# Performance work log

Measured on AMD Instinct MI355X. Metric: run time of the kernel, lower is better.

## Reference

```python
import jax, jax.numpy as jnp
import numpy as np

N = 100000
E = 1600000
F_IN = 256   # 4 * 64 after concat
H = 128

def _glorot(key, shape):
    fan_in, fan_out = shape
    lim = jnp.sqrt(6.0 / (fan_in + fan_out))
    return jax.random.uniform(key, shape, jnp.float32, -lim, lim)

def setup_inputs() -> dict:
    key = jax.random.key(0)
    ks = jax.random.split(key, 32)
    inp = {
        'x': jax.random.normal(ks[0], (N, 64), jnp.float32),
        'diff': jax.random.normal(ks[1], (N, 64), jnp.float32),
        'rec_prev': jax.random.normal(ks[2], (N, 64), jnp.float32),
        'hidden_prev': jax.random.normal(ks[3], (N, 64), jnp.float32),
        'edge_index': jax.random.randint(ks[4], (2, E), 0, N, jnp.int64),
    }
    dims = [(F_IN, H), (H, H), (H, H), (H, 1)]
    for i, (din, dout) in enumerate(dims):
        inp[f'Wl{i}'] = _glorot(ks[5 + 3 * i], (din, dout))  # neighbor (aggr) weight
        inp[f'Wr{i}'] = _glorot(ks[6 + 3 * i], (din, dout))  # root weight
        inp[f'b{i}'] = jnp.zeros((dout,), jnp.float32)
    return inp

def _sage_conv(h, src, dst, Wl, Wr, b):
    # mean aggregation of source-node features at destination nodes (PyG SAGEConv)
    msg_sum = jax.ops.segment_sum(h[src], dst, num_segments=N)        # [N, F]
    cnt = jax.ops.segment_sum(jnp.ones((src.shape[0],), h.dtype), dst, num_segments=N)
    mean = msg_sum / jnp.maximum(cnt, 1.0)[:, None]
    return mean @ Wl + h @ Wr + b

def reference(x, diff, rec_prev, hidden_prev, edge_index,
              Wl0, Wr0, b0, Wl1, Wr1, b1, Wl2, Wr2, b2, Wl3, Wr3, b3):
    src, dst = edge_index[0], edge_index[1]
    h = jnp.concatenate([x, diff, rec_prev, hidden_prev], axis=1)  # [N, 256]
    params = [(Wl0, Wr0, b0), (Wl1, Wr1, b1), (Wl2, Wr2, b2), (Wl3, Wr3, b3)]
    h = _sage_conv(h, src, dst, *params[0])
    for Wl, Wr, b in params[1:]:
        h = jax.nn.relu(h)
        h = _sage_conv(h, src, dst, Wl, Wr, b)
    out = jax.nn.sigmoid(h)          # [N, 1]
    lwp_util = jnp.mean(out)
    return out, lwp_util
```

## Files before the change

### kernel.cpp

```cpp
#include <hip/hip_runtime.h>
#include <hip/hip_bf16.h>

#define NN 100000
#define EE 1600000
#define HH 128
#define NB 391
#define CAP 5120
#define GB 1563
#define SB 256
#define EPB (EE / SB)
#define FB 6250
#define AB 6250

typedef short bf16x8 __attribute__((ext_vector_type(8)));
typedef short bf16x4 __attribute__((ext_vector_type(4)));
typedef float f32x4  __attribute__((ext_vector_type(4)));

__device__ inline short f2bf(float v) {
    __hip_bfloat16 b = __float2bfloat16(v);
    return *reinterpret_cast<short*>(&b);
}
__device__ inline float bf2f(short s) {
    unsigned int u = ((unsigned int)(unsigned short)s) << 16;
    return *reinterpret_cast<float*>(&u);
}

typedef __attribute__((address_space(1))) void gvoid_t;
typedef __attribute__((address_space(3))) void svoid_t;
__device__ __forceinline__ void gload16(const void* g, void* l) {
    __builtin_amdgcn_global_load_lds((gvoid_t*)g, (svoid_t*)l, 16, 0, 0);
}

__device__ __forceinline__ void ld_fence() { asm volatile("" ::: "memory"); }

template <int N>
__device__ __forceinline__ void wait_vm_bar() {
    if constexpr (N == 0)
        asm volatile("s_waitcnt vmcnt(0)\n\ts_barrier" ::: "memory");
    else if constexpr (N == 8)
        asm volatile("s_waitcnt vmcnt(8)\n\ts_barrier" ::: "memory");
    else if constexpr (N == 12)
        asm volatile("s_waitcnt vmcnt(12)\n\ts_barrier" ::: "memory");
    else if constexpr (N == 16)
        asm volatile("s_waitcnt vmcnt(16)\n\ts_barrier" ::: "memory");
    else if constexpr (N == 18)
        asm volatile("s_waitcnt vmcnt(18)\n\ts_barrier" ::: "memory");
    else if constexpr (N == 20)
        asm volatile("s_waitcnt vmcnt(20)\n\ts_barrier" ::: "memory");
    else
        static_assert(N == 0 || N == 8 || N == 12 || N == 16 || N == 18 || N == 20,
                      "bad N");
}
__device__ __forceinline__ void barrier_only() {
    asm volatile("s_barrier" ::: "memory");
}

__global__ __launch_bounds__(1024) void prep_kernel(
    const float* __restrict__ Wl0, const float* __restrict__ Wr0,
    const float* __restrict__ Wl1, const float* __restrict__ Wr1,
    const float* __restrict__ Wl2, const float* __restrict__ Wr2,
    __hip_bfloat16* __restrict__ WT0, __hip_bfloat16* __restrict__ WT1,
    __hip_bfloat16* __restrict__ WT2, int* __restrict__ bcur) {
    const int t = threadIdx.x;
    if (blockIdx.x == 128) {
        if (t < NB) bcur[t] = 0;
        return;
    }
    int id = blockIdx.x * 1024 + t;
    if (id < 65536) {
        int k = id & 255, n = id >> 8;
        float v = (n < 128) ? Wl0[(size_t)k * 128 + n]
                            : Wr0[(size_t)k * 128 + (n - 128)];
        WT0[(size_t)n * 256 + k] = __float2bfloat16(v);
    } else {
        id -= 65536;
        int layer = id >> 15;
        int u = id & 32767;
        int k = u & 127, n = u >> 7;
        const float* Wl = layer ? Wl2 : Wl1;
        const float* Wr = layer ? Wr2 : Wr1;
        __hip_bfloat16* WT = layer ? WT2 : WT1;
        float v = (n < 128) ? Wl[(size_t)k * 128 + n]
                            : Wr[(size_t)k * 128 + (n - 128)];
        WT[(size_t)n * 128 + k] = __float2bfloat16(v);
    }
}

#define EW 264
template <int K, bool FIRST>
__device__ __forceinline__ void gemm_body(
    short* __restrict__ lsh, int bid,
    const __hip_bfloat16* hin,
    const float* __restrict__ x0, const float* __restrict__ x1,
    const float* __restrict__ x2, const float* __restrict__ x3,
    const __hip_bfloat16* __restrict__ wt, const float* __restrict__ bias,
    __hip_bfloat16* zout, __hip_bfloat16* __restrict__ rout) {
    const int t    = threadIdx.x;
    const int w    = t >> 6;
    const int lane = t & 63;
    const int quad = lane >> 4;
    const int l16  = lane & 15;
    const int n0   = bid * 64;

    constexpr int BUFB = FIRST ? 16384 : 8192;
    char* const lc = (char*)lsh;

    const __hip_bfloat16* afeat[4];
#pragma unroll
    for (int ft = 0; ft < 4; ++ft)
        afeat[ft] = wt + (size_t)(w * 64 + ft * 16 + l16) * K + quad * 8;

    f32x4 acc[4][4];
#pragma unroll
    for (int ft = 0; ft < 4; ++ft)
#pragma unroll
        for (int nt = 0; nt < 4; ++nt)
            acc[ft][nt] = (f32x4){0.f, 0.f, 0.f, 0.f};

    bf16x8 wreg[2][8];

    auto loadW = [&](int p, int pb) {
#pragma unroll
        for (int kcl = 0; kcl < 2; ++kcl)
#pragma unroll
            for (int ft = 0; ft < 4; ++ft)
                wreg[pb][kcl * 4 + ft] =
                    *(const bf16x8*)(afeat[ft] + (p * 2 + kcl) * 32);
    };

    auto stage = [&](int p, int bb) {
        char* lb = lc + bb * BUFB;
        if constexpr (FIRST) {
            const float* sp = (p == 0) ? x0 : (p == 1) ? x1 : (p == 2) ? x2 : x3;
#pragma unroll
            for (int i = 0; i < 4; ++i) {
                const int j   = w * 4 + i;
                const int row = j * 4 + (lane >> 4);
                int rg = n0 + row; if (rg > NN - 1) rg = NN - 1;
                const int colb = ((lane & 15) * 16) ^ ((row & 15) << 4);
                gload16((const char*)sp + (size_t)rg * 256 + colb, lb + j * 1024);
            }
        } else {
#pragma unroll
            for (int i = 0; i < 2; ++i) {
                const int j   = w * 2 + i;
                const int row = j * 8 + (lane >> 3);
                int rg = n0 + row; if (rg > NN - 1) rg = NN - 1;
                const int colb = ((lane & 7) * 16) ^ ((row & 7) << 4);
                gload16((const char*)hin + (size_t)rg * 256 + p * 128 + colb,
                        lb + j * 1024);
            }
        }
    };

    auto compute = [&](int s, int bb, int pb) {
        const char* lb = lc + bb * BUFB;
#pragma unroll
        for (int kcl = 0; kcl < 2; ++kcl) {
#pragma unroll
            for (int nt = 0; nt < 4; ++nt) {
                const int row = nt * 16 + l16;
                bf16x8 b;
                if constexpr (FIRST) {
                    const int sw = (row & 15) << 4;
                    const int B0 = kcl * 128 + quad * 32;
                    const char* rb = lb + row * 256;
                    const f32x4 lo = *(const f32x4*)(rb + ((B0) ^ sw));
                    const f32x4 hi = *(const f32x4*)(rb + ((B0 + 16) ^ sw));
                    b[0] = f2bf(lo[0]); b[1] = f2bf(lo[1]);
                    b[2] = f2bf(lo[2]); b[3] = f2bf(lo[3]);
                    b[4] = f2bf(hi[0]); b[5] = f2bf(hi[1]);
                    b[6] = f2bf(hi[2]); b[7] = f2bf(hi[3]);
                } else {
                    const int sw = (row & 7) << 4;
                    const int B0 = kcl * 64 + quad * 16;
                    b = *(const bf16x8*)(lb + row * 128 + (B0 ^ sw));
                }
#pragma unroll
                for (int ft = 0; ft < 4; ++ft)
                    acc[ft][nt] = __builtin_amdgcn_mfma_f32_16x16x32_bf16(
                        wreg[pb][kcl * 4 + ft], b, acc[ft][nt], 0, 0, 0);
            }
        }
    };

    if constexpr (FIRST) {
        stage(0, 0); ld_fence();
        stage(1, 1); ld_fence();
        loadW(0, 0); ld_fence();
        wait_vm_bar<12>(); loadW(1, 1); stage(2, 2); compute(0, 0, 0); barrier_only();
        wait_vm_bar<20>(); loadW(2, 0); stage(3, 0); compute(1, 1, 1); barrier_only();
        wait_vm_bar<12>(); loadW(3, 1);              compute(2, 2, 0); barrier_only();
        wait_vm_bar<8>();                            compute(3, 0, 1); barrier_only();
    } else {
        stage(0, 0); ld_fence();
        stage(1, 1); ld_fence();
        loadW(0, 0); loadW(1, 1);
        wait_vm_bar<18>(); compute(0, 0, 0); barrier_only();
        wait_vm_bar<16>(); compute(1, 1, 1); barrier_only();
    }

#pragma unroll
    for (int ft = 0; ft < 4; ++ft) {
        const int fb = ft * 16 + quad * 4;
        float4 bv = make_float4(0.f, 0.f, 0.f, 0.f);
        if (w >= 2) bv = *(const float4*)&bias[(w - 2) * 64 + fb];
        const int cbase = (w & 1) * 64 + ((w >= 2) ? 128 : 0);
#pragma unroll
        for (int nt = 0; nt < 4; ++nt) {
            const f32x4 a = acc[ft][nt];
            bf16x4 p;
            p[0] = f2bf(a[0] + bv.x); p[1] = f2bf(a[1] + bv.y);
            p[2] = f2bf(a[2] + bv.z); p[3] = f2bf(a[3] + bv.w);
            *(bf16x4*)&lsh[(nt * 16 + l16) * EW + cbase + fb] = p;
        }
    }
    __syncthreads();
#pragma unroll
    for (int u = 0; u < 8; ++u) {
        const int id  = u * 256 + t;
        const int row = id >> 5, ch = (id & 31) * 8;
        const int nd  = n0 + row;
        if (nd < NN) {
            const bf16x8 v = *(const bf16x8*)&lsh[row * EW + ch];
            if (ch < 128) *(bf16x8*)&zout[(size_t)nd * HH + ch] = v;
            else          *(bf16x8*)&rout[(size_t)nd * HH + (ch - 128)] = v;
        }
    }
}

template <int K>
__global__ __launch_bounds__(256) void gemm_kernel(
    const __hip_bfloat16* hin,
    const __hip_bfloat16* __restrict__ wt, const float* __restrict__ bias,
    __hip_bfloat16* zout, __hip_bfloat16* __restrict__ rout) {
    __shared__ short lsh[16896];
    gemm_body<K, false>(lsh, blockIdx.x, hin, nullptr, nullptr, nullptr, nullptr,
                        wt, bias, zout, rout);
}

__global__ __launch_bounds__(256) void scatter_kernel(
    const int* __restrict__ srcv, const int* __restrict__ dstv,
    int* __restrict__ bcur, int* __restrict__ pairs) {
    __shared__ int hist[NB];
    __shared__ int base[NB];
    const int t = threadIdx.x;

    for (int j = t; j < NB; j += 256) hist[j] = 0;
    __syncthreads();

    const int e0    = blockIdx.x * EPB;
    const int eend_ = e0 + EPB;

    for (int be = e0; be < eend_; be += 4096) {
        int d[16];
#pragma unroll
        for (int u = 0; u < 16; ++u) {
            const int e = be + u * 256 + t;
            d[u] = (e < eend_) ? dstv[e] : -1;
        }
#pragma unroll
        for (int u = 0; u < 16; ++u)
            if (d[u] >= 0) atomicAdd(&hist[d[u] >> 8], 1);
    }
    __syncthreads();

    for (int j = t; j < NB; j += 256)
        base[j] = hist[j] ? atomicAdd(&bcur[j], hist[j]) : 0;
    __syncthreads();
    for (int j = t; j < NB; j += 256) hist[j] = base[j];
    __syncthreads();

    for (int be = e0; be < eend_; be += 4096) {
        int s[16], d[16];
#pragma unroll
        for (int u = 0; u < 16; ++u) {
            const int e = be + u * 256 + t;
            if (e < eend_) { s[u] = srcv[e]; d[u] = dstv[e]; }
            else d[u] = -1;
        }
#pragma unroll
        for (int u = 0; u < 16; ++u)
            if (d[u] >= 0) {
                const int b   = d[u] >> 8;
                const int pos = atomicAdd(&hist[b], 1);
                if (pos < CAP) pairs[b * CAP + pos] = (s[u] << 8) | (d[u] & 255);
            }
    }
}

__global__ __launch_bounds__(256) void fin_gemm0_kernel(
    const float* __restrict__ x0, const float* __restrict__ x1,
    const float* __restrict__ x2, const float* __restrict__ x3,
    const __hip_bfloat16* __restrict__ wt, const float* __restrict__ bias,
    __hip_bfloat16* __restrict__ zout, __hip_bfloat16* __restrict__ rout,
    const int* __restrict__ bcur, const int* __restrict__ pairs,
    int* __restrict__ csr, int* __restrict__ beg, int* __restrict__ eend,
    float* __restrict__ inv) {
    __shared__ short lsh[24576];
    const int t = threadIdx.x;

    if (blockIdx.x >= NB) {
        gemm_body<256, true>(lsh, blockIdx.x - NB, nullptr, x0, x1, x2, x3,
                             wt, bias, zout, rout);
        return;
    }

    int* cnt = (int*)lsh;
    int* scn = cnt + 256;
    int* cur = scn + 256;
    const int b = blockIdx.x;
    int m = bcur[b];
    if (m > CAP) m = CAP;

    cnt[t] = 0;
    __syncthreads();
    for (int e = t; e < m; e += 256)
        atomicAdd(&cnt[pairs[b * CAP + e] & 255], 1);
    __syncthreads();

    const int v = cnt[t];
    scn[t] = v;
    __syncthreads();
    for (int st = 1; st < 256; st <<= 1) {
        int tv = (t >= st) ? scn[t - st] : 0;
        __syncthreads();
        scn[t] += tv;
        __syncthreads();
    }
    const int myStart = scn[t] - v;
    cur[t] = myStart;
    __syncthreads();

    for (int e = t; e < m; e += 256) {
        const int pk  = pairs[b * CAP + e];
        const int pos = atomicAdd(&cur[pk & 255], 1);
        csr[b * CAP + pos] = pk >> 8;
    }

    const int node = b * 256 + t;
    if (node < NN) {
        beg[node]  = b * CAP + myStart;
        eend[node] = b * CAP + myStart + v;
        inv[node]  = 1.0f / fmaxf((float)v, 1.0f);
    }
}

template <bool LAST>
__global__ __launch_bounds__(256) void aggregate_kernel(
    const __hip_bfloat16* __restrict__ z, __hip_bfloat16* __restrict__ rio,
    const int* __restrict__ beg, const int* __restrict__ eend,
    const int* __restrict__ csr, const float* __restrict__ inv,
    const float* __restrict__ Wl3, const float* __restrict__ Wr3,
    const float* __restrict__ b3, float* __restrict__ z3,
    float* __restrict__ r3) {
    const int lane = threadIdx.x & 63;
    const int g    = lane >> 4;
    const int l16  = lane & 15;
    const int i    = ((blockIdx.x * 256 + threadIdx.x) >> 6) * 4 + g;
    if (i >= NN) return;
    const int b0 = beg[i], e0 = eend[i];
    const float iv = inv[i];
    const int  f   = l16 * 8;

    const bf16x8 rv8 = *(const bf16x8*)&rio[(size_t)i * HH + f];

    float acc[8];
#pragma unroll
    for (int j = 0; j < 8; ++j) acc[j] = 0.f;

    const size_t zoff = (size_t)f;
    int e = b0;
    for (; e + 3 < e0; e += 4) {
        const int s0 = csr[e];
        const int s1 = csr[e + 1];
        const int s2 = csr[e + 2];
        const int s3 = csr[e + 3];
        const bf16x8 z0 = *(const bf16x8*)&z[(size_t)s0 * HH + zoff];
        const bf16x8 z1 = *(const bf16x8*)&z[(size_t)s1 * HH + zoff];
        const bf16x8 z2 = *(const bf16x8*)&z[(size_t)s2 * HH + zoff];
        const bf16x8 z3v = *(const bf16x8*)&z[(size_t)s3 * HH + zoff];
#pragma unroll
        for (int j = 0; j < 8; ++j)
            acc[j] += bf2f(z0[j]) + bf2f(z1[j]) + bf2f(z2[j]) + bf2f(z3v[j]);
    }
    if (e < e0) {
        const int s0 = csr[e];
        const int s1 = (e + 1 < e0) ? csr[e + 1] : s0;
        const int s2 = (e + 2 < e0) ? csr[e + 2] : s0;
        const float m1 = (e + 1 < e0) ? 1.f : 0.f;
        const float m2 = (e + 2 < e0) ? 1.f : 0.f;
        const bf16x8 z0 = *(const bf16x8*)&z[(size_t)s0 * HH + zoff];
        const bf16x8 z1 = *(const bf16x8*)&z[(size_t)s1 * HH + zoff];
        const bf16x8 z2 = *(const bf16x8*)&z[(size_t)s2 * HH + zoff];
#pragma unroll
        for (int j = 0; j < 8; ++j) {
            acc[j] += bf2f(z0[j]);
            acc[j] = fmaf(m1, bf2f(z1[j]), acc[j]);
            acc[j] = fmaf(m2, bf2f(z2[j]), acc[j]);
        }
    }

    float ox[8];
    const __hip_bfloat162* rp = (const __hip_bfloat162*)&rv8;
#pragma unroll
    for (int j = 0; j < 4; ++j) {
        ox[2 * j]     = fmaxf(acc[2 * j]     * iv + __bfloat162float(rp[j].x), 0.f);
        ox[2 * j + 1] = fmaxf(acc[2 * j + 1] * iv + __bfloat162float(rp[j].y), 0.f);
    }

    if (!LAST) {
        bf16x8 o;
#pragma unroll
        for (int j = 0; j < 8; ++j) o[j] = f2bf(ox[j]);
        *(bf16x8*)&rio[(size_t)i * HH + f] = o;
    } else {
        const float4 wl0 = *(const float4*)&Wl3[f];
        const float4 wl1 = *(const float4*)&Wl3[f + 4];
        const float4 wr0 = *(const float4*)&Wr3[f];
        const float4 wr1 = *(const float4*)&Wr3[f + 4];
        float al = ox[0] * wl0.x + ox[1] * wl0.y + ox[2] * wl0.z + ox[3] * wl0.w
                 + ox[4] * wl1.x + ox[5] * wl1.y + ox[6] * wl1.z + ox[7] * wl1.w;
        float ar = ox[0] * wr0.x + ox[1] * wr0.y + ox[2] * wr0.z + ox[3] * wr0.w
                 + ox[4] * wr1.x + ox[5] * wr1.y + ox[6] * wr1.z + ox[7] * wr1.w;
#pragma unroll
        for (int m = 8; m; m >>= 1) {
            al += __shfl_xor(al, m, 64);
            ar += __shfl_xor(ar, m, 64);
        }
        if (l16 == 0) {
            z3[i] = al;
            r3[i] = ar + b3[0];
        }
    }
}

__global__ __launch_bounds__(256) void final_kernel(
    const float* __restrict__ z3, const float* __restrict__ r3,
    const int* __restrict__ beg, const int* __restrict__ eend,
    const int* __restrict__ csr, const float* __restrict__ inv,
    float* __restrict__ out, float* __restrict__ partial) {
    __shared__ float red[4];
    const int wv   = (blockIdx.x * 256 + threadIdx.x) >> 6;
    const int lane = threadIdx.x & 63;
    const int sub  = lane >> 4;
    const int l16  = lane & 15;
    const int w    = threadIdx.x >> 6;
    const int i    = wv * 4 + sub;
    float s = 0.f;
    if (i < NN) {
        const int b0 = beg[i], e0 = eend[i];
        float a = 0.f;
        for (int e = b0 + l16; e < e0; e += 16) a += z3[csr[e]];
        a += __shfl_xor(a, 1, 64);
        a += __shfl_xor(a, 2, 64);
        a += __shfl_xor(a, 4, 64);
        a += __shfl_xor(a, 8, 64);
        const float pre = a * inv[i] + r3[i];
        const float sg  = 1.f / (1.f + __expf(-pre));
        if (l16 == 0) { out[i] = sg; s = sg; }
    }
    s += __shfl_xor(s, 16, 64);
    s += __shfl_xor(s, 32, 64);
    if (lane == 0) red[w] = s;
    __syncthreads();
    if (threadIdx.x == 0)
        partial[blockIdx.x] = red[0] + red[1] + red[2] + red[3];
}

__global__ __launch_bounds__(256) void mean_kernel(const float* __restrict__ partial,
                                                   int nb, float* __restrict__ out) {
    __shared__ float lds[256];
    float s = 0.f;
    for (int i = threadIdx.x; i < nb; i += 256) s += partial[i];
    lds[threadIdx.x] = s;
    __syncthreads();
    for (int st = 128; st; st >>= 1) {
        if (threadIdx.x < st) lds[threadIdx.x] += lds[threadIdx.x + st];
        __syncthreads();
    }
    if (threadIdx.x == 0) out[NN] = lds[0] / (float)NN;
}

extern "C" void kernel_launch(void* const* d_in, const int* in_sizes, int n_in,
                              void* d_out, int out_size, void* d_ws, size_t ws_size,
                              hipStream_t stream) {
    const float* x    = (const float*)d_in[0];
    const float* diff = (const float*)d_in[1];
    const float* rec  = (const float*)d_in[2];
    const float* hid  = (const float*)d_in[3];
    const int* edge   = (const int*)d_in[4];
    const int* esrc = edge;
    const int* edst = edge + EE;
    const float* Wl0 = (const float*)d_in[5];
    const float* Wr0 = (const float*)d_in[6];
    const float* b0  = (const float*)d_in[7];
    const float* Wl1 = (const float*)d_in[8];
    const float* Wr1 = (const float*)d_in[9];
    const float* b1  = (const float*)d_in[10];
    const float* Wl2 = (const float*)d_in[11];
    const float* Wr2 = (const float*)d_in[12];
    const float* b2  = (const float*)d_in[13];
    const float* Wl3 = (const float*)d_in[14];
    const float* Wr3 = (const float*)d_in[15];
    const float* b3  = (const float*)d_in[16];
    float* out = (float*)d_out;

    char* w = (char*)d_ws;
    auto alloc = [&](size_t bytes) -> void* {
        void* p = (void*)w;
        w += (bytes + 255) & ~(size_t)255;
        return p;
    };
    __hip_bfloat16* bufA = (__hip_bfloat16*)alloc((size_t)NN * HH * 2);
    __hip_bfloat16* bufB = (__hip_bfloat16*)alloc((size_t)NN * HH * 2);
    __hip_bfloat16* WT0  = (__hip_bfloat16*)alloc((size_t)256 * 256 * 2);
    __hip_bfloat16* WT1  = (__hip_bfloat16*)alloc((size_t)256 * 128 * 2);
    __hip_bfloat16* WT2  = (__hip_bfloat16*)alloc((size_t)256 * 128 * 2);
    int*   pairs   = (int*)alloc((size_t)NB * CAP * 4);
    int*   csr     = (int*)alloc((size_t)NB * CAP * 4);
    int*   bcur    = (int*)alloc((size_t)512 * 4);
    int*   beg     = (int*)alloc((size_t)NN * 4);
    int*   eend    = (int*)alloc((size_t)NN * 4);
    float* inv     = (float*)alloc((size_t)NN * 4);
    float* z3      = (float*)alloc((size_t)NN * 4);
    float* r3      = (float*)alloc((size_t)NN * 4);
    float* partial = (float*)alloc((size_t)25000 * 4);

    prep_kernel<<<129, 1024, 0, stream>>>(Wl0, Wr0, Wl1, Wr1, Wl2, Wr2,
                                          WT0, WT1, WT2, bcur);

    scatter_kernel<<<SB, 256, 0, stream>>>(esrc, edst, bcur, pairs);

    fin_gemm0_kernel<<<NB + GB, 256, 0, stream>>>(
        x, diff, rec, hid, WT0, b0, bufA, bufB,
        bcur, pairs, csr, beg, eend, inv);

    aggregate_kernel<false><<<AB, 256, 0, stream>>>(bufA, bufB, beg, eend, csr, inv,
                                                    nullptr, nullptr, nullptr,
                                                    nullptr, nullptr);

    gemm_kernel<128><<<GB, 256, 0, stream>>>(bufB, WT1, b1, bufB, bufA);
    aggregate_kernel<false><<<AB, 256, 0, stream>>>(bufB, bufA, beg, eend, csr, inv,
                                                    nullptr, nullptr, nullptr,
                                                    nullptr, nullptr);

    gemm_kernel<128><<<GB, 256, 0, stream>>>(bufA, WT2, b2, bufA, bufB);
    aggregate_kernel<true><<<AB, 256, 0, stream>>>(bufA, bufB, beg, eend, csr, inv,
                                                   Wl3, Wr3, b3, z3, r3);

    final_kernel<<<FB, 256, 0, stream>>>(z3, r3, beg, eend, csr, inv, out, partial);
    mean_kernel<<<1, 256, 0, stream>>>(partial, FB, out);
}
```

Measured before the change: 454.2 us.

## Fuse prep with scatter, fold mean into final, retune gemm0 pipeline and aggregation unroll

Merges weight transposition into the scatter kernel and zeroes the bucket counters with a memset. The final kernel now computes the global mean itself, using a last-block atomic counter, which removes the separate mean launch. The first-layer GEMM loads weights before staging inputs and runs a shallower double-buffered schedule that needs less shared memory, so more blocks can be resident. The aggregation loop gathers 8 neighbors per iteration for more memory-level parallelism, at the cost of extra registers.

```diff
diff --git a/kernel.cpp b/kernel.cpp
--- a/kernel.cpp
+++ b/kernel.cpp
@@ -9,6 +9,7 @@
 #define GB 1563
 #define SB 256
 #define EPB (EE / SB)
+#define PPB 512
 #define FB 6250
 #define AB 6250
 
@@ -37,52 +38,95 @@
 __device__ __forceinline__ void wait_vm_bar() {
     if constexpr (N == 0)
         asm volatile("s_waitcnt vmcnt(0)\n\ts_barrier" ::: "memory");
-    else if constexpr (N == 8)
-        asm volatile("s_waitcnt vmcnt(8)\n\ts_barrier" ::: "memory");
+    else if constexpr (N == 4)
+        asm volatile("s_waitcnt vmcnt(4)\n\ts_barrier" ::: "memory");
     else if constexpr (N == 12)
         asm volatile("s_waitcnt vmcnt(12)\n\ts_barrier" ::: "memory");
     else if constexpr (N == 16)
         asm volatile("s_waitcnt vmcnt(16)\n\ts_barrier" ::: "memory");
     else if constexpr (N == 18)
         asm volatile("s_waitcnt vmcnt(18)\n\ts_barrier" ::: "memory");
-    else if constexpr (N == 20)
-        asm volatile("s_waitcnt vmcnt(20)\n\ts_barrier" ::: "memory");
     else
-        static_assert(N == 0 || N == 8 || N == 12 || N == 16 || N == 18 || N == 20,
-                      "bad N");
+        static_assert(N == 0 || N == 4 || N == 12 || N == 16 || N == 18, "bad N");
 }
 __device__ __forceinline__ void barrier_only() {
     asm volatile("s_barrier" ::: "memory");
 }
 
-__global__ __launch_bounds__(1024) void prep_kernel(
+__global__ __launch_bounds__(256) void prep_scatter_kernel(
     const float* __restrict__ Wl0, const float* __restrict__ Wr0,
     const float* __restrict__ Wl1, const float* __restrict__ Wr1,
     const float* __restrict__ Wl2, const float* __restrict__ Wr2,
     __hip_bfloat16* __restrict__ WT0, __hip_bfloat16* __restrict__ WT1,
-    __hip_bfloat16* __restrict__ WT2, int* __restrict__ bcur) {
+    __hip_bfloat16* __restrict__ WT2,
+    const int* __restrict__ srcv, const int* __restrict__ dstv,
+    int* __restrict__ bcur, int* __restrict__ pairs) {
+    __shared__ int hist[NB];
+    __shared__ int base[NB];
     const int t = threadIdx.x;
-    if (blockIdx.x == 128) {
-        if (t < NB) bcur[t] = 0;
+
+    if (blockIdx.x >= SB) {
+        int id = (blockIdx.x - SB) * 256 + t;
+        if (id < 65536) {
+            int k = id & 255, n = id >> 8;
+            float v = (n < 128) ? Wl0[(size_t)k * 128 + n]
+                                : Wr0[(size_t)k * 128 + (n - 128)];
+            WT0[(size_t)n * 256 + k] = __float2bfloat16(v);
+        } else {
+            id -= 65536;
+            int layer = id >> 15;
+            int u = id & 32767;
+            int k = u & 127, n = u >> 7;
+            const float* Wl = layer ? Wl2 : Wl1;
+            const float* Wr = layer ? Wr2 : Wr1;
+            __hip_bfloat16* WT = layer ? WT2 : WT1;
+            float v = (n < 128) ? Wl[(size_t)k * 128 + n]
+                                : Wr[(size_t)k * 128 + (n - 128)];
+            WT[(size_t)n * 128 + k] = __float2bfloat16(v);
+        }
         return;
     }
-    int id = blockIdx.x * 1024 + t;
-    if (id < 65536) {
-        int k = id & 255, n = id >> 8;
-        float v = (n < 128) ? Wl0[(size_t)k * 128 + n]
-                            : Wr0[(size_t)k * 128 + (n - 128)];
-        WT0[(size_t)n * 256 + k] = __float2bfloat16(v);
-    } else {
-        id -= 65536;
-        int layer = id >> 15;
-        int u = id & 32767;
-        int k = u & 127, n = u >> 7;
-        const float* Wl = layer ? Wl2 : Wl1;
-        const float* Wr = layer ? Wr2 : Wr1;
-        __hip_bfloat16* WT = layer ? WT2 : WT1;
-        float v = (n < 128) ? Wl[(size_t)k * 128 + n]
-                            : Wr[(size_t)k * 128 + (n - 128)];
-        WT[(size_t)n * 128 + k] = __float2bfloat16(v);
+
+    for (int j = t; j < NB; j += 256) hist[j] = 0;
+    __syncthreads();
+
+    const int e0    = blockIdx.x * EPB;
+    const int eend_ = e0 + EPB;
+
+    for (int be = e0; be < eend_; be += 4096) {
+        int d[16];
+#pragma unroll
+        for (int u = 0; u < 16; ++u) {
+            const int e = be + u * 256 + t;
+            d[u] = (e < eend_) ? dstv[e] : -1;
+        }
+#pragma unroll
+        for (int u = 0; u < 16; ++u)
+            if (d[u] >= 0) atomicAdd(&hist[d[u] >> 8], 1);
+    }
+    __syncthreads();
+
+    for (int j = t; j < NB; j += 256)
+        base[j] = hist[j] ? atomicAdd(&bcur[j], hist[j]) : 0;
+    __syncthreads();
+    for (int j = t; j < NB; j += 256) hist[j] = base[j];
+    __syncthreads();
+
+    for (int be = e0; be < eend_; be += 4096) {
+        int s[16], d[16];
+#pragma unroll
+        for (int u = 0; u < 16; ++u) {
+            const int e = be + u * 256 + t;
+            if (e < eend_) { s[u] = srcv[e]; d[u] = dstv[e]; }
+            else d[u] = -1;
+        }
+#pragma unroll
+        for (int u = 0; u < 16; ++u)
+            if (d[u] >= 0) {
+                const int b   = d[u] >> 8;
+                const int pos = atomicAdd(&hist[b], 1);
+                if (pos < CAP) pairs[b * CAP + pos] = (s[u] << 8) | (d[u] & 255);
+            }
     }
 }
 
@@ -185,13 +229,20 @@
     };
 
     if constexpr (FIRST) {
+        loadW(0, 0); ld_fence();
+        loadW(1, 1); ld_fence();
         stage(0, 0); ld_fence();
         stage(1, 1); ld_fence();
-        loadW(0, 0); ld_fence();
-        wait_vm_bar<12>(); loadW(1, 1); stage(2, 2); compute(0, 0, 0); barrier_only();
-        wait_vm_bar<20>(); loadW(2, 0); stage(3, 0); compute(1, 1, 1); barrier_only();
-        wait_vm_bar<12>(); loadW(3, 1);              compute(2, 2, 0); barrier_only();
-        wait_vm_bar<8>();                            compute(3, 0, 1); barrier_only();
+        wait_vm_bar<4>();
+        compute(0, 0, 0); barrier_only();
+        stage(2, 0); ld_fence(); loadW(2, 0); ld_fence();
+        wait_vm_bar<12>();
+        compute(1, 1, 1); barrier_only();
+        stage(3, 1); ld_fence(); loadW(3, 1); ld_fence();
+        wait_vm_bar<12>();
+        compute(2, 0, 0); barrier_only();
+        wait_vm_bar<0>();
+        compute(3, 1, 1); barrier_only();
     } else {
         stage(0, 0); ld_fence();
         stage(1, 1); ld_fence();
@@ -239,56 +290,6 @@
                         wt, bias, zout, rout);
 }
 
-__global__ __launch_bounds__(256) void scatter_kernel(
-    const int* __restrict__ srcv, const int* __restrict__ dstv,
-    int* __restrict__ bcur, int* __restrict__ pairs) {
-    __shared__ int hist[NB];
-    __shared__ int base[NB];
-    const int t = threadIdx.x;
-
-    for (int j = t; j < NB; j += 256) hist[j] = 0;
-    __syncthreads();
-
-    const int e0    = blockIdx.x * EPB;
-    const int eend_ = e0 + EPB;
-
-    for (int be = e0; be < eend_; be += 4096) {
-        int d[16];
-#pragma unroll
-        for (int u = 0; u < 16; ++u) {
-            const int e = be + u * 256 + t;
-            d[u] = (e < eend_) ? dstv[e] : -1;
-        }
-#pragma unroll
-        for (int u = 0; u < 16; ++u)
-            if (d[u] >= 0) atomicAdd(&hist[d[u] >> 8], 1);
-    }
-    __syncthreads();
-
-    for (int j = t; j < NB; j += 256)
-        base[j] = hist[j] ? atomicAdd(&bcur[j], hist[j]) : 0;
-    __syncthreads();
-    for (int j = t; j < NB; j += 256) hist[j] = base[j];
-    __syncthreads();
-
-    for (int be = e0; be < eend_; be += 4096) {
-        int s[16], d[16];
-#pragma unroll
-        for (int u = 0; u < 16; ++u) {
-            const int e = be + u * 256 + t;
-            if (e < eend_) { s[u] = srcv[e]; d[u] = dstv[e]; }
-            else d[u] = -1;
-        }
-#pragma unroll
-        for (int u = 0; u < 16; ++u)
-            if (d[u] >= 0) {
-                const int b   = d[u] >> 8;
-                const int pos = atomicAdd(&hist[b], 1);
-                if (pos < CAP) pairs[b * CAP + pos] = (s[u] << 8) | (d[u] & 255);
-            }
-    }
-}
-
 __global__ __launch_bounds__(256) void fin_gemm0_kernel(
     const float* __restrict__ x0, const float* __restrict__ x1,
     const float* __restrict__ x2, const float* __restrict__ x3,
@@ -297,7 +298,7 @@
     const int* __restrict__ bcur, const int* __restrict__ pairs,
     int* __restrict__ csr, int* __restrict__ beg, int* __restrict__ eend,
     float* __restrict__ inv) {
-    __shared__ short lsh[24576];
+    __shared__ short lsh[16896];
     const int t = threadIdx.x;
 
     if (blockIdx.x >= NB) {
@@ -371,18 +372,33 @@
 
     const size_t zoff = (size_t)f;
     int e = b0;
-    for (; e + 3 < e0; e += 4) {
-        const int s0 = csr[e];
-        const int s1 = csr[e + 1];
-        const int s2 = csr[e + 2];
-        const int s3 = csr[e + 3];
+    for (; e + 7 < e0; e += 8) {
+        int s[8];
+#pragma unroll
+        for (int u = 0; u < 8; ++u) s[u] = csr[e + u];
+        bf16x8 zv[8];
+#pragma unroll
+        for (int u = 0; u < 8; ++u)
+            zv[u] = *(const bf16x8*)&z[(size_t)s[u] * HH + zoff];
+#pragma unroll
+        for (int j = 0; j < 8; ++j) {
+            float a0 = bf2f(zv[0][j]) + bf2f(zv[1][j]);
+            float a1 = bf2f(zv[2][j]) + bf2f(zv[3][j]);
+            float a2 = bf2f(zv[4][j]) + bf2f(zv[5][j]);
+            float a3 = bf2f(zv[6][j]) + bf2f(zv[7][j]);
+            acc[j] += (a0 + a1) + (a2 + a3);
+        }
+    }
+    if (e + 3 < e0) {
+        const int s0 = csr[e], s1 = csr[e + 1], s2 = csr[e + 2], s3 = csr[e + 3];
         const bf16x8 z0 = *(const bf16x8*)&z[(size_t)s0 * HH + zoff];
         const bf16x8 z1 = *(const bf16x8*)&z[(size_t)s1 * HH + zoff];
         const bf16x8 z2 = *(const bf16x8*)&z[(size_t)s2 * HH + zoff];
         const bf16x8 z3v = *(const bf16x8*)&z[(size_t)s3 * HH + zoff];
 #pragma unroll
         for (int j = 0; j < 8; ++j)
-            acc[j] += bf2f(z0[j]) + bf2f(z1[j]) + bf2f(z2[j]) + bf2f(z3v[j]);
+            acc[j] += (bf2f(z0[j]) + bf2f(z1[j])) + (bf2f(z2[j]) + bf2f(z3v[j]));
+        e += 4;
     }
     if (e < e0) {
         const int s0 = csr[e];
@@ -439,8 +455,10 @@
     const float* __restrict__ z3, const float* __restrict__ r3,
     const int* __restrict__ beg, const int* __restrict__ eend,
     const int* __restrict__ csr, const float* __restrict__ inv,
-    float* __restrict__ out, float* __restrict__ partial) {
+    float* __restrict__ out, float* __restrict__ partial,
+    int* __restrict__ done) {
     __shared__ float red[4];
+    __shared__ int lastFlag;
     const int wv   = (blockIdx.x * 256 + threadIdx.x) >> 6;
     const int lane = threadIdx.x & 63;
     const int sub  = lane >> 4;
@@ -464,16 +482,19 @@
     s += __shfl_xor(s, 32, 64);
     if (lane == 0) red[w] = s;
     __syncthreads();
-    if (threadIdx.x == 0)
+    if (threadIdx.x == 0) {
         partial[blockIdx.x] = red[0] + red[1] + red[2] + red[3];
-}
-
-__global__ __launch_bounds__(256) void mean_kernel(const float* __restrict__ partial,
-                                                   int nb, float* __restrict__ out) {
+        __threadfence();
+        lastFlag = (atomicAdd(done, 1) == FB - 1);
+    }
+    __syncthreads();
+    if (!lastFlag) return;
+
+    __threadfence();
     __shared__ float lds[256];
-    float s = 0.f;
-    for (int i = threadIdx.x; i < nb; i += 256) s += partial[i];
-    lds[threadIdx.x] = s;
+    float acc = 0.f;
+    for (int j = threadIdx.x; j < FB; j += 256) acc += partial[j];
+    lds[threadIdx.x] = acc;
     __syncthreads();
     for (int st = 128; st; st >>= 1) {
         if (threadIdx.x < st) lds[threadIdx.x] += lds[threadIdx.x + st];
@@ -526,11 +547,13 @@
     float* z3      = (float*)alloc((size_t)NN * 4);
     float* r3      = (float*)alloc((size_t)NN * 4);
     float* partial = (float*)alloc((size_t)25000 * 4);
-
-    prep_kernel<<<129, 1024, 0, stream>>>(Wl0, Wr0, Wl1, Wr1, Wl2, Wr2,
-                                          WT0, WT1, WT2, bcur);
-
-    scatter_kernel<<<SB, 256, 0, stream>>>(esrc, edst, bcur, pairs);
+    int*   done    = bcur + 500;
+
+    hipMemsetAsync(bcur, 0, 512 * 4, stream);
+
+    prep_scatter_kernel<<<SB + PPB, 256, 0, stream>>>(
+        Wl0, Wr0, Wl1, Wr1, Wl2, Wr2, WT0, WT1, WT2,
+        esrc, edst, bcur, pairs);
 
     fin_gemm0_kernel<<<NB + GB, 256, 0, stream>>>(
         x, diff, rec, hid, WT0, b0, bufA, bufB,
@@ -549,6 +572,6 @@
     aggregate_kernel<true><<<AB, 256, 0, stream>>>(bufA, bufB, beg, eend, csr, inv,
                                                    Wl3, Wr3, b3, z3, r3);
 
-    final_kernel<<<FB, 256, 0, stream>>>(z3, r3, beg, eend, csr, inv, out, partial);
-    mean_kernel<<<1, 256, 0, stream>>>(partial, FB, out);
-}
+    final_kernel<<<FB, 256, 0, stream>>>(z3, r3, beg, eend, csr, inv,
+                                         out, partial, done);
+}
```

Result: slower. 576.8 us (+27.0%).
